# Kernel optimization log

Measured on AMD Instinct MI355X. Metric: run time of the kernel, lower is better.

Reference implementation:

```python
import jax, jax.numpy as jnp
import numpy as np

B, T, D = 1, 2048, 2048
NH, DH, DRH, DC = 16, 128, 64, 512


def setup_inputs() -> dict:
    key = jax.random.key(0)
    ks = jax.random.split(key, 12)
    p = lambda k, s: jax.random.normal(k, s, jnp.float32) * 0.02
    h = jax.random.normal(ks[0], (B, T, D), jnp.float32)
    # rotation angles; reference builds complex freqs_cis = cos + i*sin
    freqs_cis = jax.random.uniform(ks[1], (T, DRH // 2), jnp.float32, 0.0, 2.0 * np.pi)
    causal = jnp.tril(jnp.ones((T, T), bool))
    mask = jnp.where(causal, 0.0, -1e9).astype(jnp.float32)
    return {
        "h": h,
        "freqs_cis": freqs_cis,
        "mask": mask,
        "w_dkv": p(ks[2], (DC, D)),
        "w_uk": p(ks[3], (DH, NH, DC)),
        "w_uv": p(ks[4], (DH, NH, DC)),
        "w_dq": p(ks[5], (DC, D)),
        "w_uq": p(ks[6], (DH, NH, DC)),
        "w_qr": p(ks[7], (DRH, NH, DC)),
        "w_kr": p(ks[8], (DRH, D)),
        "w_o": p(ks[9], (D, DH, NH)),
    }


def _rope(x, fc):
    # x: [..., t, drh]; fc: complex [t, drh//2] (broadcasts over leading dims)
    real, imag = jnp.split(x.astype(jnp.float32), 2, -1)
    z = (real + 1j * imag) * fc
    return jnp.concatenate((z.real, z.imag), -1).astype(x.dtype)


def reference(h, freqs_cis, mask, w_dkv, w_uk, w_uv, w_dq, w_uq, w_qr, w_kr, w_o):
    nh, dh, drh = w_uk.shape[1], w_uk.shape[0], w_qr.shape[0]
    fc = jnp.cos(freqs_cis) + 1j * jnp.sin(freqs_cis)  # [t, drh//2] complex
    c_kv = jnp.einsum('cd,btd->btc', w_dkv, h)          # kv latent [b,t,dc]
    k_c = jnp.einsum('enc,btc->bnte', w_uk, c_kv)       # [b,nh,t,dh]
    v_c = jnp.einsum('enc,btc->bnte', w_uv, c_kv)       # [b,nh,t,dh]
    c_q = jnp.einsum('cd,btd->btc', w_dq, h)            # q latent [b,t,dc]
    q_c = jnp.einsum('enc,btc->bnte', w_uq, c_q)        # [b,nh,t,dh]
    q_r = _rope(jnp.einsum('rnc,btc->bntr', w_qr, c_q), fc)  # [b,nh,t,drh]
    k_r = _rope(jnp.einsum('rd,btd->btr', w_kr, h), fc)      # [b,t,drh]
    q = jnp.concatenate((q_c, q_r), -1)                 # [b,nh,t,dh+drh]
    b, t = k_r.shape[0], k_r.shape[1]
    k_r = jnp.broadcast_to(k_r[:, None], (b, nh, t, drh)) / nh
    k = jnp.concatenate((k_c, k_r), -1)                 # [b,nh,t,dh+drh]
    logits = jnp.einsum('bntd,bnld->bntl', q, k) / jnp.sqrt(jnp.float32(dh + drh)) + mask
    scores = jax.nn.softmax(logits.astype(jnp.float32), -1).astype(h.dtype)
    # NOTE: faithful to source: contraction is over the query axis t, output axis is l
    out = jnp.einsum('bntl,bnte->bnle', scores, v_c)    # [b,nh,t,dh] (t named l in src)
    return jnp.einsum('den,bnle->bld', w_o, out)        # [b,t,d]
```

## Files before the change

### kernel.cpp

```cpp
#include <hip/hip_runtime.h>
#include <hip/hip_bf16.h>
#include <math.h>


namespace {

constexpr int T   = 2048;
constexpr int D   = 2048;
constexpr int NH  = 16;
constexpr int DH  = 128;
constexpr int DRH = 64;
constexpr int DC  = 512;
constexpr int QK  = 192;
constexpr float SCL2E = 0.07216878364870322f * 1.4426950408889634f;

constexpr long long PH = 2048LL * 32 * 33;

typedef __attribute__((ext_vector_type(8))) short short8;
typedef __attribute__((ext_vector_type(4))) float f32x4;

#define MFMA16(a, b, c) __builtin_amdgcn_mfma_f32_16x16x32_bf16((a), (b), (c), 0, 0, 0)

__device__ __forceinline__ unsigned short f2b(float x) {
    unsigned u = __float_as_uint(x);
    unsigned r = (u + 0x7FFFu + ((u >> 16) & 1u)) >> 16;
    return (unsigned short)r;
}
__device__ __forceinline__ unsigned short f2bt(float x) {
    return (unsigned short)(__float_as_uint(x) >> 16);
}
__device__ __forceinline__ float b2f(unsigned short s) {
    return __uint_as_float(((unsigned)s) << 16);
}

typedef __attribute__((address_space(1))) const unsigned int* gas_t;
typedef __attribute__((address_space(3))) unsigned int* las_t;
__device__ __forceinline__ void async16(const unsigned short* g, unsigned short* l) {
    __builtin_amdgcn_global_load_lds((gas_t)(const void*)g, (las_t)(void*)l, 16, 0, 0);
}

constexpr long long SZ_H    = (long long)T * D;
constexpr long long SZ_DKV  = (long long)DC * D;
constexpr long long SZ_UK   = (long long)DH * NH * DC;
constexpr long long SZ_UV   = SZ_UK;
constexpr long long SZ_DQ   = SZ_DKV;
constexpr long long SZ_UQ   = SZ_UK;
constexpr long long SZ_QR   = (long long)DRH * NH * DC;
constexpr long long SZ_KR   = (long long)DRH * D;
constexpr long long C0 = SZ_H;
constexpr long long C1 = C0 + SZ_DKV;
constexpr long long C2 = C1 + SZ_UK;
constexpr long long C3 = C2 + SZ_UV;
constexpr long long C4 = C3 + SZ_DQ;
constexpr long long C5 = C4 + SZ_UQ;
constexpr long long C6 = C5 + SZ_QR;
constexpr long long C7 = C6 + SZ_KR;

__global__ __launch_bounds__(256) void cast_all(
    const float* __restrict__ h,   const float* __restrict__ wdkv,
    const float* __restrict__ wuk, const float* __restrict__ wuv,
    const float* __restrict__ wdq, const float* __restrict__ wuq,
    const float* __restrict__ wqr, const float* __restrict__ wkr,
    unsigned short* __restrict__ hb,   unsigned short* __restrict__ dkvb,
    unsigned short* __restrict__ dqb,  unsigned short* __restrict__ ukb,
    unsigned short* __restrict__ uvb,  unsigned short* __restrict__ wqall,
    unsigned short* __restrict__ krb)
{
    long long i4 = ((long long)blockIdx.x * 256 + threadIdx.x) * 4;
    const float* src; unsigned short* dst; long long soff, doff;
    if      (i4 < C0) { src = h;    dst = hb;   soff = i4;      doff = soff; }
    else if (i4 < C1) { src = wdkv; dst = dkvb; soff = i4 - C0; doff = soff; }
    else if (i4 < C2) { src = wuk;  dst = ukb;  soff = i4 - C1; doff = soff; }
    else if (i4 < C3) { src = wuv;  dst = uvb;  soff = i4 - C2; doff = soff; }
    else if (i4 < C4) { src = wdq;  dst = dqb;  soff = i4 - C3; doff = soff; }
    else if (i4 < C5) {
        src = wuq; dst = wqall; soff = i4 - C4;
        long long e = soff >> 13, n = (soff >> 9) & 15, c = soff & 511;
        doff = n * 98304 + e * 512 + c;
    }
    else if (i4 < C6) {
        src = wqr; dst = wqall; soff = i4 - C5;
        long long e = soff >> 13, n = (soff >> 9) & 15, c = soff & 511;
        doff = n * 98304 + (128 + e) * 512 + c;
    }
    else              { src = wkr;  dst = krb;  soff = i4 - C6; doff = soff; }
    float4 v = *(const float4*)(src + soff);
    uint2 pk;
    pk.x = (unsigned)f2b(v.x) | ((unsigned)f2b(v.y) << 16);
    pk.y = (unsigned)f2b(v.z) | ((unsigned)f2b(v.w) << 16);
    *(uint2*)(dst + doff) = pk;
}

__global__ __launch_bounds__(256) void wo_permute(const float* __restrict__ wo,
                                                  unsigned short* __restrict__ wob)
{
    __shared__ float row[2048];
    int d = blockIdx.x;
    const float* src = wo + (long long)d * 2048;
#pragma unroll
    for (int i = 0; i < 8; ++i) row[threadIdx.x + i * 256] = src[threadIdx.x + i * 256];
    __syncthreads();
    unsigned short* dst = wob + (long long)d * 2048;
#pragma unroll
    for (int i = 0; i < 8; ++i) {
        int j = threadIdx.x + i * 256;
        int n = j >> 7, e = j & 127;
        dst[j] = f2b(row[e * 16 + n]);
    }
}

template<int BM, int BN, int WM, int WN, bool OUTB, bool SPLITK = false>
__global__ __launch_bounds__(256) void gemm_bf16(
    const unsigned short* __restrict__ A, const unsigned short* __restrict__ B,
    void* __restrict__ C, int K, int lda, int ldb, int ldc,
    long long sB, long long sC)
{
    constexpr int MT = WM / 16, NT = WN / 16;
    constexpr int WX = BN / WN;
    __shared__ unsigned short As[2][BM * 32];
    __shared__ unsigned short Bs[2][BN * 32];
    const int tid = (int)threadIdx.x;
    const int wave = tid >> 6, lane = tid & 63;
    const int q = lane >> 4, c = lane & 15;
    const int wm = (wave / WX) * WM, wn = (wave % WX) * WN;
    const int m0 = (int)blockIdx.x * BM, n0 = (int)blockIdx.y * BN;

    const unsigned short* Ab;
    const unsigned short* Bb;
    long long cb;
    if constexpr (SPLITK) {
        int koff = (int)blockIdx.z * K;
        Ab = A + koff;
        Bb = B + koff;
        cb = (long long)blockIdx.z * sC;
    } else {
        Ab = A;
        Bb = B + (long long)blockIdx.z * sB;
        cb = (long long)blockIdx.z * sC;
    }

    f32x4 acc[MT][NT];
#pragma unroll
    for (int i = 0; i < MT; ++i)
#pragma unroll
        for (int j = 0; j < NT; ++j) acc[i][j] = (f32x4){0.f, 0.f, 0.f, 0.f};

    auto STAGE = [&](int buf, int k0) {
#pragma unroll
        for (int i = 0; i < BM / 64; ++i) {
            int ch = tid + i * 256;
            async16(&Ab[(long long)(m0 + (ch >> 2)) * lda + k0 + (((ch & 3) ^ ((ch >> 3) & 3)) * 8)],
                    &As[buf][(i * 256 + wave * 64) * 8]);
        }
#pragma unroll
        for (int i = 0; i < BN / 64; ++i) {
            int ch = tid + i * 256;
            async16(&Bb[(long long)(n0 + (ch >> 2)) * ldb + k0 + (((ch & 3) ^ ((ch >> 3) & 3)) * 8)],
                    &Bs[buf][(i * 256 + wave * 64) * 8]);
        }
    };

    STAGE(0, 0);
    __syncthreads();
    int cur = 0;
    for (int k0 = 0; k0 < K; k0 += 32) {
        if (k0 + 32 < K) STAGE(cur ^ 1, k0 + 32);
        short8 af[MT], bfr[NT];
#pragma unroll
        for (int i = 0; i < MT; ++i) {
            int row = wm + i * 16 + c;
            af[i] = *(const short8*)&As[cur][row * 32 + (q ^ ((row >> 1) & 3)) * 8];
        }
#pragma unroll
        for (int j = 0; j < NT; ++j) {
            int row = wn + j * 16 + c;
            bfr[j] = *(const short8*)&Bs[cur][row * 32 + (q ^ ((row >> 1) & 3)) * 8];
        }
#pragma unroll
        for (int i = 0; i < MT; ++i)
#pragma unroll
            for (int j = 0; j < NT; ++j)
                acc[i][j] = MFMA16(af[i], bfr[j], acc[i][j]);
        __syncthreads();
        cur ^= 1;
    }
#pragma unroll
    for (int i = 0; i < MT; ++i)
#pragma unroll
        for (int j = 0; j < NT; ++j) {
            int rbase = m0 + wm + i * 16 + q * 4;
            int col = n0 + wn + j * 16 + c;
#pragma unroll
            for (int rr = 0; rr < 4; ++rr) {
                long long off = cb + (long long)(rbase + rr) * ldc + col;
                if (OUTB) ((unsigned short*)C)[off] = f2b(acc[i][j][rr]);
                else      ((float*)C)[off] = acc[i][j][rr];
            }
        }
}

__global__ __launch_bounds__(256) void rope_q(unsigned short* __restrict__ qh,
                                              const float* __restrict__ fr)
{
    int idx = (int)blockIdx.x * 256 + (int)threadIdx.x;
    int j = idx & 31;
    int t = (idx >> 5) & (T - 1);
    int n = idx >> 16;
    float sn, cs;
    sincosf(fr[t * 32 + j], &sn, &cs);
    long long base = ((long long)(n * T + t)) * QK + 128 + j;
    float x0 = b2f(qh[base]);
    float x1 = b2f(qh[base + 32]);
    qh[base]      = f2b(x0 * cs - x1 * sn);
    qh[base + 32] = f2b(x0 * sn + x1 * cs);
}

__global__ __launch_bounds__(256) void rope_k(const float* __restrict__ krtp,
                                              unsigned short* __restrict__ kh,
                                              const float* __restrict__ fr)
{
    int idx = (int)blockIdx.x * 256 + (int)threadIdx.x;
    int j = idx & 31;
    int t = idx >> 5;
    float sn, cs;
    sincosf(fr[t * 32 + j], &sn, &cs);
    float x0 = 0.f, x1 = 0.f;
#pragma unroll
    for (int pth = 0; pth < 4; ++pth) {
        x0 += krtp[pth * (T * 64) + t * 64 + j];
        x1 += krtp[pth * (T * 64) + t * 64 + 32 + j];
    }
    unsigned short y0 = f2b((x0 * cs - x1 * sn) * (1.0f / 16.0f));
    unsigned short y1 = f2b((x0 * sn + x1 * cs) * (1.0f / 16.0f));
#pragma unroll
    for (int n = 0; n < NH; ++n) {
        long long base = ((long long)(n * T + t)) * QK + 128 + j;
        kh[base]      = y0;
        kh[base + 32] = y1;
    }
}

__global__ __launch_bounds__(256) void vtrans(const unsigned short* __restrict__ vbh,
                                              const float* __restrict__ zrow,
                                              unsigned short* __restrict__ vt)
{
    __shared__ unsigned short ts[32][33];
    __shared__ float zi[32];
    int t0 = (int)blockIdx.x * 32, e0 = (int)blockIdx.y * 32, n = (int)blockIdx.z;
    int tid = (int)threadIdx.x;
    if (tid < 32) zi[tid] = 1.0f / zrow[n * T + t0 + tid];
    int r = tid >> 3, cq = (tid & 7) * 4;
    const unsigned short* src = vbh + ((long long)(n * T + t0 + r)) * DH + e0 + cq;
#pragma unroll
    for (int i = 0; i < 4; ++i) ts[r][cq + i] = src[i];
    __syncthreads();
    unsigned short* dst = vt + ((long long)(n * DH + e0 + r)) * T + t0 + cq;
#pragma unroll
    for (int i = 0; i < 4; ++i) dst[i] = f2b(b2f(ts[cq + i][r]) * zi[cq + i]);
}

__global__ __launch_bounds__(256) void row_stats_p(const unsigned short* __restrict__ qh,
                                                   const unsigned short* __restrict__ kh,
                                                   float* __restrict__ zrow,
                                                   unsigned short* __restrict__ Pbuf)
{
    int id = (int)blockIdx.x;
    int n = (id & 7) * 2 + ((id >> 3) & 1);
    int rest = id >> 4;
    int pr = rest & 15;
    int chunk = rest >> 4;
    int tid = (int)threadIdx.x, wave = tid >> 6, lane = tid & 63;
    int q = lane >> 4, c = lane & 15;

    __shared__ unsigned short Ks[64 * 200];

    const unsigned short* kbase = kh + (long long)n * T * QK;
    unsigned short* Ph = Pbuf + (long long)n * PH;

#pragma unroll
    for (int ph = 0; ph < 2; ++ph) {
        int tbi = ph ? pr : 31 - pr;
        int tw = tbi * 64 + wave * 16;

        const unsigned short* qp = qh + ((long long)(n * T + tw + c)) * QK;
        short8 qf[6];
#pragma unroll
        for (int f = 0; f < 6; ++f) qf[f] = *(const short8*)(qp + f * 32 + q * 8);

        float z = 0.f;
        short8 kreg[6];
        int lt = chunk;
        if (lt <= tbi) {
            const unsigned short* kp = kbase + (long long)lt * 64 * QK;
#pragma unroll
            for (int i = 0; i < 6; ++i) {
                int ch = tid + i * 256;
                int r = ch / 24, cc = ch - r * 24;
                kreg[i] = *(const short8*)(kp + r * QK + cc * 8);
            }
        }
        for (; lt <= tbi; lt += 6) {
            __syncthreads();
#pragma unroll
            for (int i = 0; i < 6; ++i) {
                int ch = tid + i * 256;
                int r = ch / 24, cc = ch - r * 24;
                *(short8*)&Ks[r * 200 + cc * 8] = kreg[i];
            }
            __syncthreads();
            if (lt + 6 <= tbi) {
                const unsigned short* kp = kbase + (long long)(lt + 6) * 64 * QK;
#pragma unroll
                for (int i = 0; i < 6; ++i) {
                    int ch = tid + i * 256;
                    int r = ch / 24, cc = ch - r * 24;
                    kreg[i] = *(const short8*)(kp + r * QK + cc * 8);
                }
            }
            f32x4 d[4];
#pragma unroll
            for (int ls = 0; ls < 4; ++ls) d[ls] = (f32x4){0.f, 0.f, 0.f, 0.f};
            __builtin_amdgcn_s_setprio(1);
#pragma unroll
            for (int f = 0; f < 6; ++f)
#pragma unroll
                for (int ls = 0; ls < 4; ++ls) {
                    short8 ka = *(const short8*)&Ks[(ls * 16 + c) * 200 + f * 32 + q * 8];
                    d[ls] = MFMA16(ka, qf[f], d[ls]);
                }
            __builtin_amdgcn_s_setprio(0);
            int L = T - lt * 64;
            unsigned short* pb = Ph + (long long)2048 * lt * (65 - lt)
                                 + (long long)(q * 4) * L + (tbi - lt) * 64 + wave * 16 + c;
            if (lt == tbi) {
                int tl = wave * 16 + c;
#pragma unroll
                for (int ls = 0; ls < 4; ++ls)
#pragma unroll
                    for (int r = 0; r < 4; ++r) {
                        float pe = exp2f(d[ls][r] * SCL2E);
                        bool ok = (ls * 16 + q * 4 + r) <= tl;
                        z += ok ? pe : 0.f;
                        pb[(ls * 16 + r) * L] = ok ? f2bt(pe) : (unsigned short)0;
                    }
            } else {
#pragma unroll
                for (int ls = 0; ls < 4; ++ls)
#pragma unroll
                    for (int r = 0; r < 4; ++r) {
                        float pe = exp2f(d[ls][r] * SCL2E);
                        z += pe;
                        pb[(ls * 16 + r) * L] = f2bt(pe);
                    }
            }
        }
        z += __shfl_xor(z, 16);
        z += __shfl_xor(z, 32);
        if (q == 0) atomicAdd(&zrow[n * T + tw + c], z);
    }
}

__global__ __launch_bounds__(256) void pv_gemm(const unsigned short* __restrict__ Pbuf,
                                               const unsigned short* __restrict__ vt,
                                               unsigned short* __restrict__ p0,
                                               unsigned short* __restrict__ p1,
                                               unsigned short* __restrict__ p2,
                                               unsigned short* __restrict__ p3)
{
    __shared__ unsigned short As[2][64 * 32];
    __shared__ unsigned short Bs[2][128 * 32];
    int id = (int)blockIdx.x;
    int n = (id & 7) * 2 + ((id >> 3) & 1);
    int rest = id >> 4;
    int pr = rest & 15;
    int chunk = rest >> 4;
    const int tid = (int)threadIdx.x, wave = tid >> 6, lane = tid & 63;
    const int q = lane >> 4, c = lane & 15;
    const int wm = (wave >> 1) * 32, wn = (wave & 1) * 64;
    unsigned short* op = (chunk == 0) ? p0 : (chunk == 1) ? p1 : (chunk == 2) ? p2 : p3;

#pragma unroll
    for (int ph = 0; ph < 2; ++ph) {
        int j = ph ? (31 - pr) : pr;
        int m0 = j * 64;
        int L = T - m0;
        int ntile = 32 - j;
        const unsigned short* A = Pbuf + (long long)n * PH + (long long)2048 * j * (65 - j);
        const unsigned short* B = vt + (long long)n * DH * T + m0;

        f32x4 acc[2][4];
#pragma unroll
        for (int i = 0; i < 2; ++i)
#pragma unroll
            for (int jj = 0; jj < 4; ++jj) acc[i][jj] = (f32x4){0.f, 0.f, 0.f, 0.f};

        int tcnt = (chunk < ntile) ? (((ntile - 1 - chunk) >> 2) + 1) : 0;
        int nsteps = tcnt * 2;

        auto STAGE = [&](int buf, int k0) {
            async16(&A[(long long)(tid >> 2) * L + k0 + (((tid & 3) ^ ((tid >> 3) & 3)) * 8)],
                    &As[buf][wave * 512]);
#pragma unroll
            for (int i = 0; i < 2; ++i) {
                int ch = tid + i * 256;
                async16(&B[(long long)(ch >> 2) * T + k0 + (((ch & 3) ^ ((ch >> 3) & 3)) * 8)],
                        &Bs[buf][(i * 256 + wave * 64) * 8]);
            }
        };
        auto K0 = [&](int s) { return (chunk + ((s >> 1) << 2)) * 64 + (s & 1) * 32; };

        if (nsteps > 0) STAGE(0, K0(0));
        __syncthreads();
        int cur = 0;
        for (int s = 0; s < nsteps; ++s) {
            if (s + 1 < nsteps) STAGE(cur ^ 1, K0(s + 1));
            short8 af[2], bfr[4];
#pragma unroll
            for (int i = 0; i < 2; ++i) {
                int row = wm + i * 16 + c;
                af[i] = *(const short8*)&As[cur][row * 32 + (q ^ ((row >> 1) & 3)) * 8];
            }
#pragma unroll
            for (int jj = 0; jj < 4; ++jj) {
                int row = wn + jj * 16 + c;
                bfr[jj] = *(const short8*)&Bs[cur][row * 32 + (q ^ ((row >> 1) & 3)) * 8];
            }
#pragma unroll
            for (int i = 0; i < 2; ++i)
#pragma unroll
                for (int jj = 0; jj < 4; ++jj)
                    acc[i][jj] = MFMA16(af[i], bfr[jj], acc[i][jj]);
            __syncthreads();
            cur ^= 1;
        }
#pragma unroll
        for (int i = 0; i < 2; ++i)
#pragma unroll
            for (int jj = 0; jj < 4; ++jj) {
                int rbase = m0 + wm + i * 16 + q * 4;
                int col = n * 128 + wn + jj * 16 + c;
#pragma unroll
                for (int rr = 0; rr < 4; ++rr)
                    op[(long long)(rbase + rr) * D + col] = f2b(acc[i][jj][rr]);
            }
    }
}

__global__ __launch_bounds__(256) void sum_cast4(const unsigned short* a,
                                                 const unsigned short* b,
                                                 const unsigned short* cc_,
                                                 const unsigned short* dd_,
                                                 unsigned short* o)
{
    long long i = ((long long)blockIdx.x * 256 + threadIdx.x) * 8;
    short8 va = *(const short8*)(a + i);
    short8 vb = *(const short8*)(b + i);
    short8 vc = *(const short8*)(cc_ + i);
    short8 vd = *(const short8*)(dd_ + i);
    short8 vo;
#pragma unroll
    for (int j = 0; j < 8; ++j)
        vo[j] = (short)f2b((b2f((unsigned short)va[j]) + b2f((unsigned short)vb[j])) +
                           (b2f((unsigned short)vc[j]) + b2f((unsigned short)vd[j])));
    *(short8*)(o + i) = vo;
}

}

extern "C" void kernel_launch(void* const* d_in, const int* in_sizes, int n_in,
                              void* d_out, int out_size, void* d_ws, size_t ws_size,
                              hipStream_t stream)
{
    (void)in_sizes; (void)n_in; (void)out_size; (void)ws_size;
    const float* h    = (const float*)d_in[0];
    const float* fr   = (const float*)d_in[1];
    const float* wdkv = (const float*)d_in[3];
    const float* wuk  = (const float*)d_in[4];
    const float* wuv  = (const float*)d_in[5];
    const float* wdq  = (const float*)d_in[6];
    const float* wuq  = (const float*)d_in[7];
    const float* wqr  = (const float*)d_in[8];
    const float* wkr  = (const float*)d_in[9];
    const float* wo   = (const float*)d_in[10];
    float* out = (float*)d_out;

    char* p = (char*)d_ws;
    auto alloc = [&](long long bytes) { char* r = p; p += (bytes + 255) & ~255LL; return r; };
    unsigned short* qhb   = (unsigned short*)alloc((long long)NH * T * QK * 2);
    unsigned short* khb   = (unsigned short*)alloc((long long)NH * T * QK * 2);
    unsigned short* vbh   = (unsigned short*)alloc((long long)NH * T * DH * 2);
    float*          zrow  = (float*)alloc((long long)NH * T * 4);
    unsigned short* vtb   = (unsigned short*)alloc((long long)NH * T * DH * 2);
    unsigned short* pv3   = (unsigned short*)alloc((long long)T * D * 2);
    unsigned short* Pbuf  = (unsigned short*)alloc(PH * NH * 2);
    char* q = (char*)Pbuf;
    auto sub = [&](long long bytes) { char* r = q; q += (bytes + 255) & ~255LL; return r; };
    unsigned short* hb    = (unsigned short*)sub(SZ_H * 2);
    unsigned short* dkvb  = (unsigned short*)sub(SZ_DKV * 2);
    unsigned short* dqb   = (unsigned short*)sub(SZ_DQ * 2);
    unsigned short* ukb   = (unsigned short*)sub(SZ_UK * 2);
    unsigned short* uvb   = (unsigned short*)sub(SZ_UV * 2);
    unsigned short* wqall = (unsigned short*)sub((SZ_UQ + SZ_QR) * 2);
    unsigned short* krb   = (unsigned short*)sub(SZ_KR * 2);
    unsigned short* ckvq  = (unsigned short*)sub((long long)T * 1024 * 2);
    float*          krt   = (float*)sub((long long)T * DRH * 4 * 4);
    unsigned short* pvp0  = qhb;
    unsigned short* pvp1  = khb;
    unsigned short* pvp2  = vbh;
    unsigned short* pvp3  = pv3;
    unsigned short* attn2 = pvp0;
    unsigned short* wob   = vtb;

    cast_all<<<dim3((unsigned)(C7 / 1024)), 256, 0, stream>>>(
        h, wdkv, wuk, wuv, wdq, wuq, wqr, wkr, hb, dkvb, dqb, ukb, uvb, wqall, krb);

    gemm_bf16<64,128,32,64,true><<<dim3(T/64, 1024/128, 1), 256, 0, stream>>>(
        hb, dkvb, ckvq, D, D, D, 1024, 0, 0);
    gemm_bf16<64,64,32,32,false,true><<<dim3(T/64, 1, 4), 256, 0, stream>>>(
        hb, krb, krt, D/4, D, D, DRH, 0, (long long)T * DRH);
    gemm_bf16<64,128,32,64,true><<<dim3(T/64, 1, NH), 256, 0, stream>>>(
        ckvq, ukb, khb, DC, 1024, NH*DC, QK, DC, (long long)T * QK);
    gemm_bf16<64,128,32,64,true><<<dim3(T/64, 1, NH), 256, 0, stream>>>(
        ckvq, uvb, vbh, DC, 1024, NH*DC, DH, DC, (long long)T * DH);
    gemm_bf16<128,64,32,64,true><<<dim3(T/128, 3, NH), 256, 0, stream>>>(
        ckvq + DC, wqall, qhb, DC, 1024, DC, QK, (long long)192 * DC, (long long)T * QK);

    rope_q<<<dim3(NH * T * 32 / 256), 256, 0, stream>>>(qhb, fr);
    rope_k<<<dim3(T * 32 / 256), 256, 0, stream>>>(krt, khb, fr);

    hipMemsetAsync(zrow, 0, (long long)NH * T * 4, stream);
    row_stats_p<<<dim3(1536), 256, 0, stream>>>(qhb, khb, zrow, Pbuf);
    vtrans<<<dim3(T/32, DH/32, NH), 256, 0, stream>>>(vbh, zrow, vtb);
    pv_gemm<<<dim3(1024), 256, 0, stream>>>(Pbuf, vtb, pvp0, pvp1, pvp2, pvp3);
    sum_cast4<<<dim3(T * D / 2048), 256, 0, stream>>>(pvp0, pvp1, pvp2, pvp3, attn2);

    wo_permute<<<dim3(D), 256, 0, stream>>>(wo, wob);
    gemm_bf16<64,128,32,64,false><<<dim3(T/64, D/128, 1), 256, 0, stream>>>(
        attn2, wob, out, D, D, D, D, 0, 0);
}
```

Baseline: 322.1 us.

## Stage P tiles through LDS for coalesced stores and retile waves 2x2

The row_stats_p kernel now has each wave compute a 32x32 sub-tile (2x2 MFMA blocks) instead of 16x64. This lets each K fragment loaded from LDS feed two MFMAs. The exponentiated P values are written into an LDS staging tile and then stored to global memory as contiguous 16-byte vectors, replacing the scattered 2-byte strided stores. The grid shrinks from 1536 to 1024 blocks with a chunk stride of 4, and launch bounds request 4 blocks per CU. This adds an extra barrier per tile and more LDS per block.

```diff
diff --git a/kernel.cpp b/kernel.cpp
--- a/kernel.cpp
+++ b/kernel.cpp
@@ -259,10 +259,10 @@
     for (int i = 0; i < 4; ++i) dst[i] = f2b(b2f(ts[cq + i][r]) * zi[cq + i]);
 }
 
-__global__ __launch_bounds__(256) void row_stats_p(const unsigned short* __restrict__ qh,
-                                                   const unsigned short* __restrict__ kh,
-                                                   float* __restrict__ zrow,
-                                                   unsigned short* __restrict__ Pbuf)
+__global__ __launch_bounds__(256, 4) void row_stats_p(const unsigned short* __restrict__ qh,
+                                                      const unsigned short* __restrict__ kh,
+                                                      float* __restrict__ zrow,
+                                                      unsigned short* __restrict__ Pbuf)
 {
     int id = (int)blockIdx.x;
     int n = (id & 7) * 2 + ((id >> 3) & 1);
@@ -271,36 +271,42 @@
     int chunk = rest >> 4;
     int tid = (int)threadIdx.x, wave = tid >> 6, lane = tid & 63;
     int q = lane >> 4, c = lane & 15;
+    int wl = wave >> 1, wt = wave & 1;
 
     __shared__ unsigned short Ks[64 * 200];
+    __shared__ unsigned short Pt[64 * 72];
 
     const unsigned short* kbase = kh + (long long)n * T * QK;
     unsigned short* Ph = Pbuf + (long long)n * PH;
 
+    auto PREF = [&](short8* kreg, int lt) {
+        const unsigned short* kp = kbase + (long long)lt * 64 * QK;
+#pragma unroll
+        for (int i = 0; i < 6; ++i) {
+            int ch = tid + i * 256;
+            int r = ch / 24, cc = ch - r * 24;
+            kreg[i] = *(const short8*)(kp + r * QK + cc * 8);
+        }
+    };
+
 #pragma unroll
     for (int ph = 0; ph < 2; ++ph) {
         int tbi = ph ? pr : 31 - pr;
-        int tw = tbi * 64 + wave * 16;
-
-        const unsigned short* qp = qh + ((long long)(n * T + tw + c)) * QK;
-        short8 qf[6];
-#pragma unroll
-        for (int f = 0; f < 6; ++f) qf[f] = *(const short8*)(qp + f * 32 + q * 8);
-
-        float z = 0.f;
+        int tw = tbi * 64 + wt * 32;
+
+        short8 qf[6][2];
+#pragma unroll
+        for (int jj = 0; jj < 2; ++jj) {
+            const unsigned short* qp = qh + ((long long)(n * T + tw + jj * 16 + c)) * QK;
+#pragma unroll
+            for (int f = 0; f < 6; ++f) qf[f][jj] = *(const short8*)(qp + f * 32 + q * 8);
+        }
+
+        float z[2] = {0.f, 0.f};
         short8 kreg[6];
         int lt = chunk;
-        if (lt <= tbi) {
-            const unsigned short* kp = kbase + (long long)lt * 64 * QK;
-#pragma unroll
-            for (int i = 0; i < 6; ++i) {
-                int ch = tid + i * 256;
-                int r = ch / 24, cc = ch - r * 24;
-                kreg[i] = *(const short8*)(kp + r * QK + cc * 8);
-            }
-        }
-        for (; lt <= tbi; lt += 6) {
-            __syncthreads();
+        if (lt <= tbi) PREF(kreg, lt);
+        for (; lt <= tbi; lt += 4) {
 #pragma unroll
             for (int i = 0; i < 6; ++i) {
                 int ch = tid + i * 256;
@@ -308,55 +314,74 @@
                 *(short8*)&Ks[r * 200 + cc * 8] = kreg[i];
             }
             __syncthreads();
-            if (lt + 6 <= tbi) {
-                const unsigned short* kp = kbase + (long long)(lt + 6) * 64 * QK;
-#pragma unroll
-                for (int i = 0; i < 6; ++i) {
-                    int ch = tid + i * 256;
-                    int r = ch / 24, cc = ch - r * 24;
-                    kreg[i] = *(const short8*)(kp + r * QK + cc * 8);
-                }
-            }
-            f32x4 d[4];
-#pragma unroll
-            for (int ls = 0; ls < 4; ++ls) d[ls] = (f32x4){0.f, 0.f, 0.f, 0.f};
+            if (lt + 4 <= tbi) PREF(kreg, lt + 4);
+            f32x4 d[2][2];
+#pragma unroll
+            for (int ii = 0; ii < 2; ++ii)
+#pragma unroll
+                for (int jj = 0; jj < 2; ++jj) d[ii][jj] = (f32x4){0.f, 0.f, 0.f, 0.f};
             __builtin_amdgcn_s_setprio(1);
 #pragma unroll
-            for (int f = 0; f < 6; ++f)
-#pragma unroll
-                for (int ls = 0; ls < 4; ++ls) {
-                    short8 ka = *(const short8*)&Ks[(ls * 16 + c) * 200 + f * 32 + q * 8];
-                    d[ls] = MFMA16(ka, qf[f], d[ls]);
-                }
+            for (int f = 0; f < 6; ++f) {
+                short8 ka0 = *(const short8*)&Ks[(wl * 32 + c) * 200 + f * 32 + q * 8];
+                short8 ka1 = *(const short8*)&Ks[(wl * 32 + 16 + c) * 200 + f * 32 + q * 8];
+                d[0][0] = MFMA16(ka0, qf[f][0], d[0][0]);
+                d[0][1] = MFMA16(ka0, qf[f][1], d[0][1]);
+                d[1][0] = MFMA16(ka1, qf[f][0], d[1][0]);
+                d[1][1] = MFMA16(ka1, qf[f][1], d[1][1]);
+            }
             __builtin_amdgcn_s_setprio(0);
-            int L = T - lt * 64;
-            unsigned short* pb = Ph + (long long)2048 * lt * (65 - lt)
-                                 + (long long)(q * 4) * L + (tbi - lt) * 64 + wave * 16 + c;
+            int br = wl * 32 + q * 4;
+            int bt = wt * 32 + c;
             if (lt == tbi) {
-                int tl = wave * 16 + c;
-#pragma unroll
-                for (int ls = 0; ls < 4; ++ls)
-#pragma unroll
-                    for (int r = 0; r < 4; ++r) {
-                        float pe = exp2f(d[ls][r] * SCL2E);
-                        bool ok = (ls * 16 + q * 4 + r) <= tl;
-                        z += ok ? pe : 0.f;
-                        pb[(ls * 16 + r) * L] = ok ? f2bt(pe) : (unsigned short)0;
+#pragma unroll
+                for (int ii = 0; ii < 2; ++ii)
+#pragma unroll
+                    for (int jj = 0; jj < 2; ++jj) {
+                        int tl = bt + jj * 16;
+#pragma unroll
+                        for (int r = 0; r < 4; ++r) {
+                            float pe = exp2f(d[ii][jj][r] * SCL2E);
+                            int ll = br + ii * 16 + r;
+                            bool ok = ll <= tl;
+                            z[jj] += ok ? pe : 0.f;
+                            Pt[ll * 72 + tl] = ok ? f2bt(pe) : (unsigned short)0;
+                        }
                     }
             } else {
 #pragma unroll
-                for (int ls = 0; ls < 4; ++ls)
-#pragma unroll
-                    for (int r = 0; r < 4; ++r) {
-                        float pe = exp2f(d[ls][r] * SCL2E);
-                        z += pe;
-                        pb[(ls * 16 + r) * L] = f2bt(pe);
+                for (int ii = 0; ii < 2; ++ii)
+#pragma unroll
+                    for (int jj = 0; jj < 2; ++jj) {
+                        int tl = bt + jj * 16;
+#pragma unroll
+                        for (int r = 0; r < 4; ++r) {
+                            float pe = exp2f(d[ii][jj][r] * SCL2E);
+                            z[jj] += pe;
+                            Pt[(br + ii * 16 + r) * 72 + tl] = f2bt(pe);
+                        }
                     }
             }
-        }
-        z += __shfl_xor(z, 16);
-        z += __shfl_xor(z, 32);
-        if (q == 0) atomicAdd(&zrow[n * T + tw + c], z);
+            __syncthreads();
+            int row = tid >> 2;
+            int cs = (tid & 3) * 8;
+            int L = T - lt * 64;
+            unsigned short* gb = Ph + (long long)2048 * lt * (65 - lt)
+                                 + (long long)row * L + (tbi - lt) * 64;
+            short8 v0 = *(const short8*)&Pt[row * 72 + cs];
+            short8 v1 = *(const short8*)&Pt[row * 72 + cs + 32];
+            *(short8*)(gb + cs) = v0;
+            *(short8*)(gb + cs + 32) = v1;
+        }
+#pragma unroll
+        for (int jj = 0; jj < 2; ++jj) {
+            z[jj] += __shfl_xor(z[jj], 16);
+            z[jj] += __shfl_xor(z[jj], 32);
+        }
+        if (q == 0) {
+            atomicAdd(&zrow[n * T + tw + c], z[0]);
+            atomicAdd(&zrow[n * T + tw + 16 + c], z[1]);
+        }
     }
 }
 
@@ -529,7 +554,7 @@
     rope_k<<<dim3(T * 32 / 256), 256, 0, stream>>>(krt, khb, fr);
 
     hipMemsetAsync(zrow, 0, (long long)NH * T * 4, stream);
-    row_stats_p<<<dim3(1536), 256, 0, stream>>>(qhb, khb, zrow, Pbuf);
+    row_stats_p<<<dim3(1024), 256, 0, stream>>>(qhb, khb, zrow, Pbuf);
     vtrans<<<dim3(T/32, DH/32, NH), 256, 0, stream>>>(vbh, zrow, vtb);
     pv_gemm<<<dim3(1024), 256, 0, stream>>>(Pbuf, vtb, pvp0, pvp1, pvp2, pvp3);
     sum_cast4<<<dim3(T * D / 2048), 256, 0, stream>>>(pvp0, pvp1, pvp2, pvp3, attn2);
```

After: 385.8 us. +19.8%, slower.
